# Optimization experiments

Measured on AMD Instinct MI355X. Metric: run time of the kernel, lower is better.

Reference implementation:

```python
import jax, jax.numpy as jnp
import numpy as np

B, S, K, V, H = 32, 2048, 512, 512, 256


def setup_inputs() -> dict:
    key = jax.random.key(0)
    ks = jax.random.split(key, 6)
    r = 0.1  # init_range
    return {
        "q": jax.random.normal(ks[0], (B, K), jnp.float32),
        "k": jax.random.normal(ks[1], (S, B, K), jnp.float32),
        "v": jax.random.normal(ks[2], (S, B, V), jnp.float32),
        "Wk": jax.random.uniform(ks[3], (H, K), jnp.float32, -r, r),
        "bk": jnp.zeros((H,), jnp.float32),
        "Wq": jax.random.uniform(ks[4], (H, K), jnp.float32, -r, r),
        "bq": jnp.zeros((H,), jnp.float32),
        "Wo": jax.random.uniform(ks[5], (1, H), jnp.float32, -r, r),
        "bo": jnp.zeros((1,), jnp.float32),
    }


def reference(q, k, v, Wk, bk, Wq, bq, Wo, bo):
    # k, v: [S, B, *] -> batch-first [B, S, *]
    kb = jnp.transpose(k, (1, 0, 2))  # [B, S, K]
    vb = jnp.transpose(v, (1, 0, 2))  # [B, S, V]
    h_k = jnp.einsum('bsk,hk->bsh', kb, Wk) + bk        # key2hid
    h_q = q @ Wq.T + bq                                  # [B, H]
    h = jnp.tanh(h_k + h_q[:, None, :])                  # [B, S, H]
    logit = jnp.einsum('bsh,h->bs', h, Wo[0]) + bo[0]    # hid2output, squeeze
    logit = logit - jnp.max(logit, axis=1, keepdims=True)
    p = jax.nn.softmax(logit, axis=1)                    # [B, S]
    out = jnp.sum(vb * p[:, :, None], axis=1, keepdims=True)  # [B, 1, V]
    out = jnp.transpose(out, (1, 0, 2))                  # [1, B, V]
    return out, p
```

## Files before the change

### kernel.cpp

```cpp
#include <hip/hip_runtime.h>
#include <stdint.h>

#define Bb 32
#define Ss 2048
#define Kk 512
#define Vv 512
#define Hh 256

#define OUTP (Bb * Vv)

#define WS_HQ 0
#define WS_WKB 32768
#define WS_LOGIT 294912

typedef float floatx4 __attribute__((ext_vector_type(4)));
typedef __bf16 bf16x8 __attribute__((ext_vector_type(8)));

__device__ __forceinline__ uint32_t bfround(float f) {
  uint32_t u = __float_as_uint(f);
  return (u + 0x7fffu + ((u >> 16) & 1u)) >> 16;
}
__device__ __forceinline__ uint32_t packbf(float lo, float hi) {
  return bfround(lo) | (bfround(hi) << 16);
}

__device__ __forceinline__ void gload_lds16(const uint16_t* g, uint16_t* l) {
  __builtin_amdgcn_global_load_lds((const __attribute__((address_space(1))) void*)g,
                                   (__attribute__((address_space(3))) void*)l, 16, 0, 0);
}

__global__ void prep(const float* __restrict__ q, const float* __restrict__ Wq,
                     const float* __restrict__ bq, const float* __restrict__ bk,
                     const float* __restrict__ Wk, uint16_t* __restrict__ wkb,
                     float* __restrict__ hq, float* __restrict__ dout) {
  __shared__ float red[256];
  const int bx = blockIdx.x;
  const int t = threadIdx.x;
  if (bx < 128) {
    const int i = (bx * 256 + t) * 4;
    float4 w = *(const float4*)(Wk + i);
    const int h = i >> 9;
    const int k = i & 511;
    const int stage = k >> 5;
    const int grp = (k & 31) >> 3;
    const int j = k & 7;
    uint2 pk;
    pk.x = packbf(w.x, w.y);
    pk.y = packbf(w.z, w.w);
    *(uint2*)(wkb + stage * 8192 + (grp * 256 + h) * 8 + j) = pk;
  } else if (bx < 384) {
    const int idx = bx - 128;
    const int b = idx >> 3;
    const int hc = idx & 7;
    const int h_in = t & 31;
    const int kp = t >> 5;
    const int h = hc * 32 + h_in;
    const float4* qp = (const float4*)(q + b * Kk + kp * 64);
    const float4* wp = (const float4*)(Wq + h * Kk + kp * 64);
    float acc = 0.f;
#pragma unroll
    for (int i = 0; i < 16; ++i) {
      float4 qa = qp[i], wa = wp[i];
      acc = fmaf(qa.x, wa.x, acc);
      acc = fmaf(qa.y, wa.y, acc);
      acc = fmaf(qa.z, wa.z, acc);
      acc = fmaf(qa.w, wa.w, acc);
    }
    red[t] = acc;
    __syncthreads();
    if (t < 32) {
      float s = 0.f;
#pragma unroll
      for (int kp2 = 0; kp2 < 8; ++kp2) s += red[kp2 * 32 + t];
      const int hh = hc * 32 + t;
      hq[b * Hh + hh] = s + bq[hh] + bk[hh];
    }
  } else {
    float4 z = {0.f, 0.f, 0.f, 0.f};
    float4* o = (float4*)dout + t;
#pragma unroll
    for (int i = 0; i < 16; ++i) o[i * 256] = z;
  }
}

__global__ __launch_bounds__(256, 4) void fused_gemm_tanh_logit(
    const float* __restrict__ kin, const uint16_t* __restrict__ wkb,
    const float* __restrict__ hq, const float* __restrict__ Wo,
    float* __restrict__ wlog, const float* __restrict__ vin,
    float* __restrict__ dout) {
  __shared__ __align__(16) uint16_t lA[2][2048];
  __shared__ __align__(16) uint16_t lB[2][8192];

  const int tid = threadIdx.x;
  const int sc = blockIdx.x;
  const int b = blockIdx.y;
  const int wid = tid >> 6;
  const int lane = tid & 63;
  const int l15 = lane & 15;
  const int lg = lane >> 4;

  float hqv[4], wov[4];
#pragma unroll
  for (int ni = 0; ni < 4; ++ni) {
    const int n = wid * 64 + ni * 16 + l15;
    hqv[ni] = hq[b * Hh + n];
    wov[ni] = Wo[n];
  }

  floatx4 acc[4][4];
#pragma unroll
  for (int mi = 0; mi < 4; ++mi)
#pragma unroll
    for (int ni = 0; ni < 4; ++ni) acc[mi][ni] = (floatx4){0.f, 0.f, 0.f, 0.f};

  const int arow = tid >> 2;
  const int apart = tid & 3;
  const float* aptr = kin + ((size_t)((sc * 64 + arow) * Bb) + b) * Kk + apart * 8;
  uint16_t* awr = &lA[0][0] + (apart * 64 + arow) * 8;

  const uint16_t* bsrc = wkb + (wid * 4) * 512 + lane * 8;
  uint16_t* bdst = &lB[0][0] + (wid * 4) * 512;

  float4 av0, av1;

#pragma unroll
  for (int it = 0; it < 4; ++it) gload_lds16(bsrc + it * 512, bdst + it * 512);
  {
    float4 a0 = *(const float4*)(aptr);
    float4 a1 = *(const float4*)(aptr + 4);
    av0 = *(const float4*)(aptr + 32);
    av1 = *(const float4*)(aptr + 36);
    uint4 w;
    w.x = packbf(a0.x, a0.y);
    w.y = packbf(a0.z, a0.w);
    w.z = packbf(a1.x, a1.y);
    w.w = packbf(a1.z, a1.w);
    *(uint4*)awr = w;
  }
  __syncthreads();

#pragma unroll
  for (int ks = 0; ks < 16; ++ks) {
    const int cur = ks & 1, nxt = cur ^ 1;
    if (ks < 15) {
#pragma unroll
      for (int it = 0; it < 4; ++it)
        gload_lds16(bsrc + (ks + 1) * 8192 + it * 512, bdst + nxt * 8192 + it * 512);
    }
    if (ks < 15) {
      uint4 w;
      w.x = packbf(av0.x, av0.y);
      w.y = packbf(av0.z, av0.w);
      w.z = packbf(av1.x, av1.y);
      w.w = packbf(av1.z, av1.w);
      *(uint4*)(awr + nxt * 2048) = w;
    }
    if (ks < 14) {
      av0 = *(const float4*)(aptr + (ks + 2) * 32);
      av1 = *(const float4*)(aptr + (ks + 2) * 32 + 4);
    }
    {
      bf16x8 af[4], bfr[4];
#pragma unroll
      for (int mi = 0; mi < 4; ++mi)
        af[mi] = *(const bf16x8*)&lA[cur][(lg * 64 + mi * 16 + l15) * 8];
#pragma unroll
      for (int ni = 0; ni < 4; ++ni)
        bfr[ni] = *(const bf16x8*)&lB[cur][(lg * 256 + wid * 64 + ni * 16 + l15) * 8];
#pragma unroll
      for (int mi = 0; mi < 4; ++mi)
#pragma unroll
        for (int ni = 0; ni < 4; ++ni)
          acc[mi][ni] = __builtin_amdgcn_mfma_f32_16x16x32_bf16(
              af[mi], bfr[ni], acc[mi][ni], 0, 0, 0);
    }
    if (ks < 15) __syncthreads();
  }

  float* lpart = (float*)&lA[0][0];
  float* sw = (float*)&lA[0][0] + 256;
#pragma unroll
  for (int mi = 0; mi < 4; ++mi) {
#pragma unroll
    for (int r = 0; r < 4; ++r) {
      float sum = 0.f;
#pragma unroll
      for (int ni = 0; ni < 4; ++ni) {
        const float x = acc[mi][ni][r] + hqv[ni];
        const float e = __expf(2.f * x);
        const float th = 1.f - 2.f * __builtin_amdgcn_rcpf(e + 1.f);
        sum = fmaf(th, wov[ni], sum);
      }
      sum += __shfl_xor(sum, 1, 64);
      sum += __shfl_xor(sum, 2, 64);
      sum += __shfl_xor(sum, 4, 64);
      sum += __shfl_xor(sum, 8, 64);
      if (l15 == 0) lpart[wid * 64 + mi * 16 + lg * 4 + r] = sum;
    }
  }
  __syncthreads();
  if (tid < 64) {
    const float lv = lpart[tid] + lpart[64 + tid] + lpart[128 + tid] + lpart[192 + tid];
    const float w = __expf(lv);
    wlog[b * Ss + sc * 64 + tid] = w;
    sw[tid] = w;
  }
  __syncthreads();

  const int c = tid * 2;
  float ax = 0.f, ay = 0.f;
#pragma unroll 8
  for (int s = 0; s < 64; ++s) {
    const float2 vv = *(const float2*)(vin + ((size_t)((sc * 64 + s) * Bb) + b) * Vv + c);
    const float pw = sw[s];
    ax = fmaf(pw, vv.x, ax);
    ay = fmaf(pw, vv.y, ay);
  }
  float* o = dout + b * Vv + c;
  atomicAdd(o + 0, ax);
  atomicAdd(o + 1, ay);
}

__global__ void finalize(const float* __restrict__ wlog, float* __restrict__ dout) {
  const int b = blockIdx.x;
  const int t = threadIdx.x;
  const int wid = t >> 6, lane = t & 63;
  __shared__ float red[4];
  const float4* wp = (const float4*)(wlog + b * Ss);
  const float4 x0 = wp[t * 2], x1 = wp[t * 2 + 1];
  float s = ((x0.x + x0.y) + (x0.z + x0.w)) + ((x1.x + x1.y) + (x1.z + x1.w));
#pragma unroll
  for (int off = 1; off < 64; off <<= 1) s += __shfl_xor(s, off, 64);
  if (lane == 0) red[wid] = s;
  __syncthreads();
  s = (red[0] + red[1]) + (red[2] + red[3]);
  const float inv = 1.f / s;
  float4 p0, p1;
  p0.x = x0.x * inv; p0.y = x0.y * inv; p0.z = x0.z * inv; p0.w = x0.w * inv;
  p1.x = x1.x * inv; p1.y = x1.y * inv; p1.z = x1.z * inv; p1.w = x1.w * inv;
  float4* pout = (float4*)(dout + OUTP + b * Ss);
  pout[t * 2] = p0;
  pout[t * 2 + 1] = p1;
  float2* op = (float2*)(dout + b * Vv + t * 2);
  float2 ov = *op;
  ov.x *= inv;
  ov.y *= inv;
  *op = ov;
}

extern "C" void kernel_launch(void* const* d_in, const int* in_sizes, int n_in,
                              void* d_out, int out_size, void* d_ws, size_t ws_size,
                              hipStream_t stream) {
  const float* q  = (const float*)d_in[0];
  const float* k  = (const float*)d_in[1];
  const float* v  = (const float*)d_in[2];
  const float* Wk = (const float*)d_in[3];
  const float* bk = (const float*)d_in[4];
  const float* Wq = (const float*)d_in[5];
  const float* bq = (const float*)d_in[6];
  const float* Wo = (const float*)d_in[7];

  float* out = (float*)d_out;
  char* ws = (char*)d_ws;
  float* hq = (float*)(ws + WS_HQ);
  uint16_t* wkb = (uint16_t*)(ws + WS_WKB);
  float* wlog = (float*)(ws + WS_LOGIT);

  prep<<<dim3(385), dim3(256), 0, stream>>>(q, Wq, bq, bk, Wk, wkb, hq, out);
  fused_gemm_tanh_logit<<<dim3(Ss / 64, Bb), dim3(256), 0, stream>>>(k, wkb, hq, Wo, wlog, v, out);
  finalize<<<dim3(Bb), dim3(256), 0, stream>>>(wlog, out);
}
```

Before: 299.7 us.

## Load GEMM operands directly from global into registers, drop LDS staging

Removes the double-buffered LDS staging of the k tile and bf16 Wk tile. Each wave now loads its MFMA fragments straight from global memory into registers and converts them to bf16 there, which eliminates the per-step barriers and LDS writes and reads. Each of the four waves now reads the same A rows separately, so global and L2 traffic for k goes up. Launch bounds drop from 4 to 3 blocks per SM, and the v reduction switches to float4 loads split across two s-halves, which doubles the atomics per output element.

```diff
diff --git a/kernel.cpp b/kernel.cpp
--- a/kernel.cpp
+++ b/kernel.cpp
@@ -22,11 +22,6 @@
 }
 __device__ __forceinline__ uint32_t packbf(float lo, float hi) {
   return bfround(lo) | (bfround(hi) << 16);
-}
-
-__device__ __forceinline__ void gload_lds16(const uint16_t* g, uint16_t* l) {
-  __builtin_amdgcn_global_load_lds((const __attribute__((address_space(1))) void*)g,
-                                   (__attribute__((address_space(3))) void*)l, 16, 0, 0);
 }
 
 __global__ void prep(const float* __restrict__ q, const float* __restrict__ Wq,
@@ -83,13 +78,13 @@
   }
 }
 
-__global__ __launch_bounds__(256, 4) void fused_gemm_tanh_logit(
+__global__ __launch_bounds__(256, 3) void fused_gemm_tanh_logit(
     const float* __restrict__ kin, const uint16_t* __restrict__ wkb,
     const float* __restrict__ hq, const float* __restrict__ Wo,
     float* __restrict__ wlog, const float* __restrict__ vin,
     float* __restrict__ dout) {
-  __shared__ __align__(16) uint16_t lA[2][2048];
-  __shared__ __align__(16) uint16_t lB[2][8192];
+  __shared__ float lpart[256];
+  __shared__ float sw[64];
 
   const int tid = threadIdx.x;
   const int sc = blockIdx.x;
@@ -113,72 +108,52 @@
 #pragma unroll
     for (int ni = 0; ni < 4; ++ni) acc[mi][ni] = (floatx4){0.f, 0.f, 0.f, 0.f};
 
-  const int arow = tid >> 2;
-  const int apart = tid & 3;
-  const float* aptr = kin + ((size_t)((sc * 64 + arow) * Bb) + b) * Kk + apart * 8;
-  uint16_t* awr = &lA[0][0] + (apart * 64 + arow) * 8;
-
-  const uint16_t* bsrc = wkb + (wid * 4) * 512 + lane * 8;
-  uint16_t* bdst = &lB[0][0] + (wid * 4) * 512;
-
-  float4 av0, av1;
-
-#pragma unroll
-  for (int it = 0; it < 4; ++it) gload_lds16(bsrc + it * 512, bdst + it * 512);
-  {
-    float4 a0 = *(const float4*)(aptr);
-    float4 a1 = *(const float4*)(aptr + 4);
-    av0 = *(const float4*)(aptr + 32);
-    av1 = *(const float4*)(aptr + 36);
-    uint4 w;
-    w.x = packbf(a0.x, a0.y);
-    w.y = packbf(a0.z, a0.w);
-    w.z = packbf(a1.x, a1.y);
-    w.w = packbf(a1.z, a1.w);
-    *(uint4*)awr = w;
-  }
-  __syncthreads();
-
-#pragma unroll
+  const float* ap0 = kin + ((size_t)((sc * 64 + 0 * 16 + l15) * Bb) + b) * Kk + lg * 8;
+  const float* ap1 = kin + ((size_t)((sc * 64 + 1 * 16 + l15) * Bb) + b) * Kk + lg * 8;
+  const float* ap2 = kin + ((size_t)((sc * 64 + 2 * 16 + l15) * Bb) + b) * Kk + lg * 8;
+  const float* ap3 = kin + ((size_t)((sc * 64 + 3 * 16 + l15) * Bb) + b) * Kk + lg * 8;
+
+  const uint16_t* bp = wkb + ((size_t)(lg * 256 + wid * 64 + l15)) * 8;
+
+#pragma unroll 4
   for (int ks = 0; ks < 16; ++ks) {
-    const int cur = ks & 1, nxt = cur ^ 1;
-    if (ks < 15) {
-#pragma unroll
-      for (int it = 0; it < 4; ++it)
-        gload_lds16(bsrc + (ks + 1) * 8192 + it * 512, bdst + nxt * 8192 + it * 512);
-    }
-    if (ks < 15) {
+    bf16x8 bfr[4];
+#pragma unroll
+    for (int ni = 0; ni < 4; ++ni)
+      bfr[ni] = *(const bf16x8*)(bp + (size_t)ks * 8192 + ni * 128);
+    bf16x8 af[4];
+    {
+      float4 p0, p1;
       uint4 w;
-      w.x = packbf(av0.x, av0.y);
-      w.y = packbf(av0.z, av0.w);
-      w.z = packbf(av1.x, av1.y);
-      w.w = packbf(av1.z, av1.w);
-      *(uint4*)(awr + nxt * 2048) = w;
-    }
-    if (ks < 14) {
-      av0 = *(const float4*)(aptr + (ks + 2) * 32);
-      av1 = *(const float4*)(aptr + (ks + 2) * 32 + 4);
-    }
-    {
-      bf16x8 af[4], bfr[4];
-#pragma unroll
-      for (int mi = 0; mi < 4; ++mi)
-        af[mi] = *(const bf16x8*)&lA[cur][(lg * 64 + mi * 16 + l15) * 8];
+      p0 = *(const float4*)(ap0 + ks * 32);
+      p1 = *(const float4*)(ap0 + ks * 32 + 4);
+      w.x = packbf(p0.x, p0.y); w.y = packbf(p0.z, p0.w);
+      w.z = packbf(p1.x, p1.y); w.w = packbf(p1.z, p1.w);
+      af[0] = __builtin_bit_cast(bf16x8, w);
+      p0 = *(const float4*)(ap1 + ks * 32);
+      p1 = *(const float4*)(ap1 + ks * 32 + 4);
+      w.x = packbf(p0.x, p0.y); w.y = packbf(p0.z, p0.w);
+      w.z = packbf(p1.x, p1.y); w.w = packbf(p1.z, p1.w);
+      af[1] = __builtin_bit_cast(bf16x8, w);
+      p0 = *(const float4*)(ap2 + ks * 32);
+      p1 = *(const float4*)(ap2 + ks * 32 + 4);
+      w.x = packbf(p0.x, p0.y); w.y = packbf(p0.z, p0.w);
+      w.z = packbf(p1.x, p1.y); w.w = packbf(p1.z, p1.w);
+      af[2] = __builtin_bit_cast(bf16x8, w);
+      p0 = *(const float4*)(ap3 + ks * 32);
+      p1 = *(const float4*)(ap3 + ks * 32 + 4);
+      w.x = packbf(p0.x, p0.y); w.y = packbf(p0.z, p0.w);
+      w.z = packbf(p1.x, p1.y); w.w = packbf(p1.z, p1.w);
+      af[3] = __builtin_bit_cast(bf16x8, w);
+    }
+#pragma unroll
+    for (int mi = 0; mi < 4; ++mi)
 #pragma unroll
       for (int ni = 0; ni < 4; ++ni)
-        bfr[ni] = *(const bf16x8*)&lB[cur][(lg * 256 + wid * 64 + ni * 16 + l15) * 8];
-#pragma unroll
-      for (int mi = 0; mi < 4; ++mi)
-#pragma unroll
-        for (int ni = 0; ni < 4; ++ni)
-          acc[mi][ni] = __builtin_amdgcn_mfma_f32_16x16x32_bf16(
-              af[mi], bfr[ni], acc[mi][ni], 0, 0, 0);
-    }
-    if (ks < 15) __syncthreads();
-  }
-
-  float* lpart = (float*)&lA[0][0];
-  float* sw = (float*)&lA[0][0] + 256;
+        acc[mi][ni] = __builtin_amdgcn_mfma_f32_16x16x32_bf16(
+            af[mi], bfr[ni], acc[mi][ni], 0, 0, 0);
+  }
+
 #pragma unroll
   for (int mi = 0; mi < 4; ++mi) {
 #pragma unroll
@@ -207,18 +182,24 @@
   }
   __syncthreads();
 
-  const int c = tid * 2;
-  float ax = 0.f, ay = 0.f;
+  const int c4 = tid & 127;
+  const int sh = tid >> 7;
+  float4 a4 = {0.f, 0.f, 0.f, 0.f};
 #pragma unroll 8
-  for (int s = 0; s < 64; ++s) {
-    const float2 vv = *(const float2*)(vin + ((size_t)((sc * 64 + s) * Bb) + b) * Vv + c);
+  for (int i = 0; i < 32; ++i) {
+    const int s = sh + 2 * i;
+    const float4 vv = *(const float4*)(vin + ((size_t)((sc * 64 + s) * Bb) + b) * Vv + c4 * 4);
     const float pw = sw[s];
-    ax = fmaf(pw, vv.x, ax);
-    ay = fmaf(pw, vv.y, ay);
-  }
-  float* o = dout + b * Vv + c;
-  atomicAdd(o + 0, ax);
-  atomicAdd(o + 1, ay);
+    a4.x = fmaf(pw, vv.x, a4.x);
+    a4.y = fmaf(pw, vv.y, a4.y);
+    a4.z = fmaf(pw, vv.z, a4.z);
+    a4.w = fmaf(pw, vv.w, a4.w);
+  }
+  float* o = dout + b * Vv + c4 * 4;
+  atomicAdd(o + 0, a4.x);
+  atomicAdd(o + 1, a4.y);
+  atomicAdd(o + 2, a4.z);
+  atomicAdd(o + 3, a4.w);
 }
 
 __global__ void finalize(const float* __restrict__ wlog, float* __restrict__ dout) {
```

Result: slower. 398.5 us (+33.0%).
